# Performance work log

Measured on AMD Instinct MI355X. Metric: run time of the kernel, lower is better.

Reference implementation:

```python
import jax, jax.numpy as jnp
import numpy as np

BETA = 1.0
POWER_ITERS = 9
EPS = 1e-12  # F.normalize default eps


def _normalize(v):
    # L2 normalize over dim=1 of [B, N, 1], matching F.normalize(x, dim=1)
    n = jnp.linalg.norm(v, axis=1, keepdims=True)
    return v / jnp.maximum(n, EPS)


def _dominant_eigenvalue(A, x):
    # A: [B, N, N], x: [B, N, 1]
    for _ in range(POWER_ITERS):
        x = _normalize(jnp.matmul(A, x))
    Ax = jnp.matmul(A, x)[..., 0]              # [B, N]
    num = jnp.sum(Ax * x[..., 0], axis=1)      # x^T A x
    den = jnp.sum(x[..., 0] ** 2, axis=1)      # ||x||^2 (== 1 after normalize)
    return num / den, x


def setup_inputs() -> dict:
    key = jax.random.key(0)
    k1, k2 = jax.random.split(key)
    B, C, H, W = 256, 2048, 7, 7
    x = jax.random.normal(k1, (B, C, H, W), dtype=jnp.float32)
    x0 = _normalize(jax.random.normal(k2, (B, H * W, 1), dtype=jnp.float32))
    return {"x": x, "x0": x0}


def reference(x, x0):
    B, C, H, W = x.shape
    N = H * W
    Wm = x.reshape(B, C, N)
    # ATA = W^T W : [B, N, N]
    ATA = jnp.einsum('bcn,bcm->bnm', Wm, Wm)
    # first power iteration: largest eigenvalue; x0 is a no_grad constant
    largest, x1 = _dominant_eigenvalue(ATA, jax.lax.stop_gradient(x0))
    I = jnp.eye(N, dtype=ATA.dtype)
    shifted = ATA - largest[:, None, None] * I
    # second power iteration warm-started from detached x1 (torch stores last_x detached)
    tmp, _ = _dominant_eigenvalue(shifted, jax.lax.stop_gradient(x1))
    smallest = tmp + largest
    penalty = BETA * (largest / smallest - 1.0) ** 2
    return jnp.sum(penalty) / B
```

## Files before the change

kernel.cpp:

```cpp
#include <hip/hip_runtime.h>
#include <hip/hip_bf16.h>
#include <stdint.h>


#define BATCH 256
#define CDIM  2048
#define NDIM  49
#define QK    512
#define NQ    4
#define CHUNK 64
#define NCHUNK (QK / CHUNK)
#define CHUNK_FLOATS (CHUNK * NDIM)
#define CHUNK_F4 (CHUNK_FLOATS / 4)
#define CPAD (CHUNK_FLOATS + 16)
#define PSIZE (NDIM * NDIM)
#define ASTRIDE 53

typedef __bf16 bf16x8 __attribute__((ext_vector_type(8)));
typedef float  f32x16 __attribute__((ext_vector_type(16)));

__device__ inline void async_load16(const float* g, float* l) {
  __builtin_amdgcn_global_load_lds(
      (const __attribute__((address_space(1))) void*)g,
      (__attribute__((address_space(3))) void*)l,
      16 , 0 , 0 );
}

__global__ __launch_bounds__(256, 4) void gram_kernel(
    const float* __restrict__ x, float* __restrict__ partial,
    float* __restrict__ out) {
  __shared__ float raw[2][CPAD];

  const int tid  = threadIdx.x;
  const int bidx = blockIdx.x;
  const int batch = bidx >> 2;
  const int q     = bidx & 3;
  const int lane = tid & 63;
  const int wv   = tid >> 6;
  const int ln   = lane & 31;
  const int hf   = lane >> 5;
  const int qm   = wv >> 1, qn = wv & 1;
  const int m = qm * 32 + ln;
  const int n = qn * 32 + ln;

  if (bidx == 0 && tid == 0) out[0] = 0.f;

  const float* gbase = x + (size_t)batch * (CDIM * NDIM)
                         + (size_t)q * (QK * NDIM);

  f32x16 c1, c2, c3;
#pragma unroll
  for (int i = 0; i < 16; ++i) { c1[i] = 0.f; c2[i] = 0.f; c3[i] = 0.f; }

#pragma unroll
  for (int i = 0; i < (CHUNK_F4 + 255) / 256; ++i) {
    int slot = i * 256 + tid;
    if (slot < CHUNK_F4) async_load16(gbase + slot * 4, &raw[0][slot * 4]);
  }

  for (int ch = 0; ch < NCHUNK; ++ch) {
    __syncthreads();
    const int cur = ch & 1;
    if (ch + 1 < NCHUNK) {
      const float* gch = gbase + (ch + 1) * CHUNK_FLOATS;
      float* dst = raw[cur ^ 1];
#pragma unroll
      for (int i = 0; i < (CHUNK_F4 + 255) / 256; ++i) {
        int slot = i * 256 + tid;
        if (slot < CHUNK_F4) async_load16(gch + slot * 4, &dst[slot * 4]);
      }
    }

    const float* buf = raw[cur];
#pragma unroll
    for (int s = 0; s < CHUNK / 16; ++s) {
      const int kk = s * 16 + hf * 8;
      const float* pa = &buf[kk * NDIM + m];
      const float* pb = &buf[kk * NDIM + n];
      bf16x8 ah, al, bh, bl;
#pragma unroll
      for (int j = 0; j < 8; ++j) {
        float av = pa[j * NDIM];
        __bf16 h = (__bf16)av;
        ah[j] = h;
        al[j] = (__bf16)(av - (float)h);
        float bv = pb[j * NDIM];
        __bf16 hb = (__bf16)bv;
        bh[j] = hb;
        bl[j] = (__bf16)(bv - (float)hb);
      }
      c1 = __builtin_amdgcn_mfma_f32_32x32x16_bf16(ah, bh, c1, 0, 0, 0);
      c2 = __builtin_amdgcn_mfma_f32_32x32x16_bf16(ah, bl, c2, 0, 0, 0);
      c3 = __builtin_amdgcn_mfma_f32_32x32x16_bf16(al, bh, c3, 0, 0, 0);
    }
  }

  float* outp = partial + (size_t)bidx * PSIZE;
#pragma unroll
  for (int r = 0; r < 16; ++r) {
    int row = (r & 3) + 8 * (r >> 2) + 4 * hf;
    int mm = qm * 32 + row;
    if (mm < NDIM && n < NDIM)
      outp[mm * NDIM + n] = c1[r] + c2[r] + c3[r];
  }
}

__global__ __launch_bounds__(64) void eigen_kernel(
    const float* __restrict__ partial, const float* __restrict__ x0,
    float* __restrict__ out) {
  __shared__ float A[NDIM * ASTRIDE];
  __shared__ float xv[64];

  const int b = blockIdx.x;
  const int t = threadIdx.x;
  const float* p0 = partial + (size_t)(NQ * b) * PSIZE;

  for (int idx = t; idx < NDIM * NDIM; idx += 64) {
    int r = idx / NDIM;
    int c = idx - r * NDIM;
    float v = 0.f;
#pragma unroll
    for (int qq = 0; qq < NQ; ++qq) v += p0[qq * PSIZE + idx];
    A[r * ASTRIDE + c] = v;
  }
  if (t < NDIM) xv[t] = x0[b * NDIM + t];
  __syncthreads();

  auto rayleigh_power = [&](float shift) -> float {
    for (int it = 0; it < 9; ++it) {
      float y = 0.f;
      if (t < NDIM) {
        const float* Ar = &A[t * ASTRIDE];
#pragma unroll 7
        for (int k = 0; k < NDIM; ++k) y = fmaf(Ar[k], xv[k], y);
        y -= shift * xv[t];
      }
      float s = y * y;
#pragma unroll
      for (int o = 32; o; o >>= 1) s += __shfl_xor(s, o, 64);
      float nrm = fmaxf(sqrtf(s), 1e-12f);
      __syncthreads();
      if (t < NDIM) xv[t] = y / nrm;
      __syncthreads();
    }
    float yy = 0.f;
    if (t < NDIM) {
      const float* Ar = &A[t * ASTRIDE];
#pragma unroll 7
      for (int k = 0; k < NDIM; ++k) yy = fmaf(Ar[k], xv[k], yy);
      yy -= shift * xv[t];
    }
    float num = (t < NDIM) ? yy * xv[t] : 0.f;
    float den = (t < NDIM) ? xv[t] * xv[t] : 0.f;
#pragma unroll
    for (int o = 32; o; o >>= 1) {
      num += __shfl_xor(num, o, 64);
      den += __shfl_xor(den, o, 64);
    }
    return num / den;
  };

  float largest = rayleigh_power(0.f);
  float tmp = rayleigh_power(largest);
  float smallest = tmp + largest;

  if (t == 0) {
    float r = largest / smallest - 1.f;
    atomicAdd(out, r * r * (1.0f / (float)BATCH));
  }
}

extern "C" void kernel_launch(void* const* d_in, const int* in_sizes, int n_in,
                              void* d_out, int out_size, void* d_ws,
                              size_t ws_size, hipStream_t stream) {
  const float* x  = (const float*)d_in[0];
  const float* x0 = (const float*)d_in[1];
  float* out = (float*)d_out;
  float* partial = (float*)d_ws;

  gram_kernel<<<1024, 256, 0, stream>>>(x, partial, out);
  eigen_kernel<<<BATCH, 64, 0, stream>>>(partial, x0, out);
}
```

Measured before the change: 178.9 us.

## Pre-convert Gram inputs to swizzled bf16 hi/lo LDS tiles and register-cache eigen rows

The Gram kernel now loads each chunk into registers, splits it into bf16 high and low parts once per element, and stores them in XOR-swizzled LDS buffers. The MFMA loop then reads 16-byte vectors instead of converting scalar floats from LDS per wave, which removes redundant conversions and strided LDS reads. The eigen kernel pads the partial stride so it can reduce with vector loads, runs 256 threads per block (all four waves compute redundantly), holds each matrix row in registers, and splits the dot product across four accumulators. The trade-offs are higher register pressure, loss of the async global-to-LDS copy overlap, and the four-accumulator split slightly changes float summation order.

```diff
diff --git a/kernel.cpp b/kernel.cpp
--- a/kernel.cpp
+++ b/kernel.cpp
@@ -10,26 +10,65 @@
 #define NQ    4
 #define CHUNK 64
 #define NCHUNK (QK / CHUNK)
-#define CHUNK_FLOATS (CHUNK * NDIM)
-#define CHUNK_F4 (CHUNK_FLOATS / 4)
-#define CPAD (CHUNK_FLOATS + 16)
-#define PSIZE (NDIM * NDIM)
-#define ASTRIDE 53
+#define ITEMS (NDIM * (CHUNK / 8))
+#define PSTRIDE 2404
 
 typedef __bf16 bf16x8 __attribute__((ext_vector_type(8)));
 typedef float  f32x16 __attribute__((ext_vector_type(16)));
-
-__device__ inline void async_load16(const float* g, float* l) {
-  __builtin_amdgcn_global_load_lds(
-      (const __attribute__((address_space(1))) void*)g,
-      (__attribute__((address_space(3))) void*)l,
-      16 , 0 , 0 );
+typedef float  f32x4  __attribute__((ext_vector_type(4)));
+
+union V16 {
+  f32x4  f4;
+  bf16x8 b8;
+};
+
+__device__ __forceinline__ void load8(const float* __restrict__ g,
+                                      float (&r)[8]) {
+#pragma unroll
+  for (int j = 0; j < 8; ++j) r[j] = g[j * NDIM];
+}
+
+__device__ __forceinline__ void cvt_store(const float (&r)[8], uint32_t* Hb,
+                                          uint32_t* Lb, int w) {
+  bf16x8 hv, lv;
+#pragma unroll
+  for (int j = 0; j < 8; ++j) {
+    float e = r[j];
+    __bf16 h = (__bf16)e;
+    hv[j] = h;
+    lv[j] = (__bf16)(e - (float)h);
+  }
+  V16 a, b;
+  a.b8 = hv;
+  b.b8 = lv;
+  *(f32x4*)(Hb + w) = a.f4;
+  *(f32x4*)(Lb + w) = b.f4;
+}
+
+__device__ __forceinline__ void comp16(const uint32_t* Hb, const uint32_t* Lb,
+                                       int m, int n, int hf, f32x16& c1,
+                                       f32x16& c2, f32x16& c3) {
+  const f32x4* H = (const f32x4*)Hb;
+  const f32x4* L = (const f32x4*)Lb;
+#pragma unroll
+  for (int s = 0; s < 4; ++s) {
+    const int blk = 2 * s + hf;
+    V16 ah, al, bh, bl;
+    ah.f4 = H[m * 8 + (blk ^ (m & 7))];
+    al.f4 = L[m * 8 + (blk ^ (m & 7))];
+    bh.f4 = H[n * 8 + (blk ^ (n & 7))];
+    bl.f4 = L[n * 8 + (blk ^ (n & 7))];
+    c1 = __builtin_amdgcn_mfma_f32_32x32x16_bf16(ah.b8, bh.b8, c1, 0, 0, 0);
+    c2 = __builtin_amdgcn_mfma_f32_32x32x16_bf16(ah.b8, bl.b8, c2, 0, 0, 0);
+    c3 = __builtin_amdgcn_mfma_f32_32x32x16_bf16(al.b8, bh.b8, c3, 0, 0, 0);
+  }
 }
 
 __global__ __launch_bounds__(256, 4) void gram_kernel(
     const float* __restrict__ x, float* __restrict__ partial,
     float* __restrict__ out) {
-  __shared__ float raw[2][CPAD];
+  __shared__ __align__(16) uint32_t ldsHi[2][2048];
+  __shared__ __align__(16) uint32_t ldsLo[2][2048];
 
   const int tid  = threadIdx.x;
   const int bidx = blockIdx.x;
@@ -39,7 +78,7 @@
   const int wv   = tid >> 6;
   const int ln   = lane & 31;
   const int hf   = lane >> 5;
-  const int qm   = wv >> 1, qn = wv & 1;
+  const int qm = wv >> 1, qn = wv & 1;
   const int m = qm * 32 + ln;
   const int n = qn * 32 + ln;
 
@@ -48,54 +87,51 @@
   const float* gbase = x + (size_t)batch * (CDIM * NDIM)
                          + (size_t)q * (QK * NDIM);
 
+  const int i0 = tid;
+  const int i1 = tid + 256;
+  const bool v1 = (i1 < ITEMS);
+  const int kq0 = (i0 * 1338) >> 16;
+  const int n0  = i0 - 49 * kq0;
+  const int kq1 = (i1 * 1338) >> 16;
+  const int n1  = i1 - 49 * kq1;
+  const int g0  = kq0 * (8 * NDIM) + n0;
+  const int g1  = kq1 * (8 * NDIM) + n1;
+  const int w0  = n0 * 32 + 4 * (kq0 ^ (n0 & 7));
+  const int w1  = n1 * 32 + 4 * (kq1 ^ (n1 & 7));
+
   f32x16 c1, c2, c3;
 #pragma unroll
   for (int i = 0; i < 16; ++i) { c1[i] = 0.f; c2[i] = 0.f; c3[i] = 0.f; }
 
-#pragma unroll
-  for (int i = 0; i < (CHUNK_F4 + 255) / 256; ++i) {
-    int slot = i * 256 + tid;
-    if (slot < CHUNK_F4) async_load16(gbase + slot * 4, &raw[0][slot * 4]);
-  }
-
-  for (int ch = 0; ch < NCHUNK; ++ch) {
+  float sA0[8], sA1[8], sB0[8], sB1[8];
+
+  load8(gbase + g0, sA0);
+  if (v1) load8(gbase + g1, sA1);
+
+#pragma unroll
+  for (int ch = 0; ch < NCHUNK; ch += 2) {
+    {
+      const float* gch = gbase + (size_t)(ch + 1) * (CHUNK * NDIM);
+      load8(gch + g0, sB0);
+      if (v1) load8(gch + g1, sB1);
+    }
+    cvt_store(sA0, ldsHi[0], ldsLo[0], w0);
+    if (v1) cvt_store(sA1, ldsHi[0], ldsLo[0], w1);
     __syncthreads();
-    const int cur = ch & 1;
-    if (ch + 1 < NCHUNK) {
-      const float* gch = gbase + (ch + 1) * CHUNK_FLOATS;
-      float* dst = raw[cur ^ 1];
-#pragma unroll
-      for (int i = 0; i < (CHUNK_F4 + 255) / 256; ++i) {
-        int slot = i * 256 + tid;
-        if (slot < CHUNK_F4) async_load16(gch + slot * 4, &dst[slot * 4]);
-      }
-    }
-
-    const float* buf = raw[cur];
-#pragma unroll
-    for (int s = 0; s < CHUNK / 16; ++s) {
-      const int kk = s * 16 + hf * 8;
-      const float* pa = &buf[kk * NDIM + m];
-      const float* pb = &buf[kk * NDIM + n];
-      bf16x8 ah, al, bh, bl;
-#pragma unroll
-      for (int j = 0; j < 8; ++j) {
-        float av = pa[j * NDIM];
-        __bf16 h = (__bf16)av;
-        ah[j] = h;
-        al[j] = (__bf16)(av - (float)h);
-        float bv = pb[j * NDIM];
-        __bf16 hb = (__bf16)bv;
-        bh[j] = hb;
-        bl[j] = (__bf16)(bv - (float)hb);
-      }
-      c1 = __builtin_amdgcn_mfma_f32_32x32x16_bf16(ah, bh, c1, 0, 0, 0);
-      c2 = __builtin_amdgcn_mfma_f32_32x32x16_bf16(ah, bl, c2, 0, 0, 0);
-      c3 = __builtin_amdgcn_mfma_f32_32x32x16_bf16(al, bh, c3, 0, 0, 0);
-    }
-  }
-
-  float* outp = partial + (size_t)bidx * PSIZE;
+    comp16(ldsHi[0], ldsLo[0], m, n, hf, c1, c2, c3);
+
+    if (ch + 2 < NCHUNK) {
+      const float* gch = gbase + (size_t)(ch + 2) * (CHUNK * NDIM);
+      load8(gch + g0, sA0);
+      if (v1) load8(gch + g1, sA1);
+    }
+    cvt_store(sB0, ldsHi[1], ldsLo[1], w0);
+    if (v1) cvt_store(sB1, ldsHi[1], ldsLo[1], w1);
+    __syncthreads();
+    comp16(ldsHi[1], ldsLo[1], m, n, hf, c1, c2, c3);
+  }
+
+  float* outp = partial + (size_t)bidx * PSTRIDE;
 #pragma unroll
   for (int r = 0; r < 16; ++r) {
     int row = (r & 3) + 8 * (r >> 2) + 4 * hf;
@@ -105,53 +141,74 @@
   }
 }
 
-__global__ __launch_bounds__(64) void eigen_kernel(
+__global__ __launch_bounds__(256) void eigen_kernel(
     const float* __restrict__ partial, const float* __restrict__ x0,
     float* __restrict__ out) {
-  __shared__ float A[NDIM * ASTRIDE];
-  __shared__ float xv[64];
-
-  const int b = blockIdx.x;
-  const int t = threadIdx.x;
-  const float* p0 = partial + (size_t)(NQ * b) * PSIZE;
-
-  for (int idx = t; idx < NDIM * NDIM; idx += 64) {
-    int r = idx / NDIM;
-    int c = idx - r * NDIM;
-    float v = 0.f;
-#pragma unroll
-    for (int qq = 0; qq < NQ; ++qq) v += p0[qq * PSIZE + idx];
-    A[r * ASTRIDE + c] = v;
-  }
+  __shared__ __align__(16) float A[NDIM * NDIM + 3];
+  __shared__ float xv[NDIM];
+
+  const int b  = blockIdx.x;
+  const int t  = threadIdx.x;
+  const int ln = t & 63;
+  const float* p0 = partial + (size_t)(NQ * b) * PSTRIDE;
+
+  const f32x4* q0 = (const f32x4*)(p0);
+  const f32x4* q1 = (const f32x4*)(p0 + PSTRIDE);
+  const f32x4* q2 = (const f32x4*)(p0 + 2 * PSTRIDE);
+  const f32x4* q3 = (const f32x4*)(p0 + 3 * PSTRIDE);
+  for (int i = t; i < 600; i += 256) {
+    f32x4 s = q0[i] + q1[i] + q2[i] + q3[i];
+    ((f32x4*)A)[i] = s;
+  }
+  if (t == 0)
+    A[2400] = p0[2400] + p0[PSTRIDE + 2400] + p0[2 * PSTRIDE + 2400] +
+              p0[3 * PSTRIDE + 2400];
   if (t < NDIM) xv[t] = x0[b * NDIM + t];
   __syncthreads();
 
-  auto rayleigh_power = [&](float shift) -> float {
+  float Ar[NDIM];
+  {
+    const float* Arow = &A[((ln < NDIM) ? ln : (NDIM - 1)) * NDIM];
+#pragma unroll
+    for (int k = 0; k < NDIM; ++k) Ar[k] = Arow[k];
+  }
+  const bool act = (ln < NDIM);
+
+  auto rayleigh = [&](float shift) -> float {
     for (int it = 0; it < 9; ++it) {
-      float y = 0.f;
-      if (t < NDIM) {
-        const float* Ar = &A[t * ASTRIDE];
-#pragma unroll 7
-        for (int k = 0; k < NDIM; ++k) y = fmaf(Ar[k], xv[k], y);
-        y -= shift * xv[t];
+      float a0 = 0.f, a1 = 0.f, a2 = 0.f, a3 = 0.f;
+#pragma unroll
+      for (int k = 0; k < 48; k += 4) {
+        a0 = fmaf(Ar[k + 0], xv[k + 0], a0);
+        a1 = fmaf(Ar[k + 1], xv[k + 1], a1);
+        a2 = fmaf(Ar[k + 2], xv[k + 2], a2);
+        a3 = fmaf(Ar[k + 3], xv[k + 3], a3);
       }
-      float s = y * y;
-#pragma unroll
-      for (int o = 32; o; o >>= 1) s += __shfl_xor(s, o, 64);
-      float nrm = fmaxf(sqrtf(s), 1e-12f);
+      a0 = fmaf(Ar[48], xv[48], a0);
+      float xvl = act ? xv[ln] : 0.f;
+      float y = act ? (((a0 + a1) + (a2 + a3)) - shift * xvl) : 0.f;
+      float s2 = y * y;
+#pragma unroll
+      for (int o = 32; o; o >>= 1) s2 += __shfl_xor(s2, o, 64);
+      float nrm = fmaxf(sqrtf(s2), 1e-12f);
+      float xn = y / nrm;
       __syncthreads();
-      if (t < NDIM) xv[t] = y / nrm;
+      if (t < NDIM) xv[t] = xn;
       __syncthreads();
     }
-    float yy = 0.f;
-    if (t < NDIM) {
-      const float* Ar = &A[t * ASTRIDE];
-#pragma unroll 7
-      for (int k = 0; k < NDIM; ++k) yy = fmaf(Ar[k], xv[k], yy);
-      yy -= shift * xv[t];
-    }
-    float num = (t < NDIM) ? yy * xv[t] : 0.f;
-    float den = (t < NDIM) ? xv[t] * xv[t] : 0.f;
+    float a0 = 0.f, a1 = 0.f, a2 = 0.f, a3 = 0.f;
+#pragma unroll
+    for (int k = 0; k < 48; k += 4) {
+      a0 = fmaf(Ar[k + 0], xv[k + 0], a0);
+      a1 = fmaf(Ar[k + 1], xv[k + 1], a1);
+      a2 = fmaf(Ar[k + 2], xv[k + 2], a2);
+      a3 = fmaf(Ar[k + 3], xv[k + 3], a3);
+    }
+    a0 = fmaf(Ar[48], xv[48], a0);
+    float xvl = act ? xv[ln] : 0.f;
+    float yy = act ? (((a0 + a1) + (a2 + a3)) - shift * xvl) : 0.f;
+    float num = yy * xvl;
+    float den = xvl * xvl;
 #pragma unroll
     for (int o = 32; o; o >>= 1) {
       num += __shfl_xor(num, o, 64);
@@ -160,8 +217,8 @@
     return num / den;
   };
 
-  float largest = rayleigh_power(0.f);
-  float tmp = rayleigh_power(largest);
+  float largest  = rayleigh(0.f);
+  float tmp      = rayleigh(largest);
   float smallest = tmp + largest;
 
   if (t == 0) {
@@ -179,5 +236,5 @@
   float* partial = (float*)d_ws;
 
   gram_kernel<<<1024, 256, 0, stream>>>(x, partial, out);
-  eigen_kernel<<<BATCH, 64, 0, stream>>>(partial, x0, out);
-}
+  eigen_kernel<<<BATCH, 256, 0, stream>>>(partial, x0, out);
+}
```

New measurement: 169.4 us. -5.4%, faster.
